# Performance work log

Measured on AMD Instinct MI355X. Metric: run time of the kernel, lower is better.

## Reference

```python
import jax, jax.numpy as jnp
import numpy as np

N_NODES = 50000
EPS = 1e-5


def sage_conv_max(x, src, dst, W_l, b_l, W_r):
    # PyG SAGEConv(aggr='max'): out = lin_l(max_j x_j) + lin_r(x_i)
    msg = x[src]                                   # [E, d] gather
    agg = jnp.full((x.shape[0], x.shape[1]), -jnp.inf, dtype=x.dtype)
    agg = agg.at[dst].max(msg)                     # scatter-max over edges
    agg = jnp.where(jnp.isneginf(agg), 0.0, agg)   # isolated nodes -> 0 (PyG convention)
    return agg @ W_l.T + b_l + x @ W_r.T


def batch_norm(x, gamma, beta):
    mean = jnp.mean(x, axis=0)
    var = jnp.var(x, axis=0)
    return (x - mean) * jax.lax.rsqrt(var + EPS) * gamma + beta


def setup_inputs() -> dict:
    key = jax.random.key(0)
    ks = jax.random.split(key, 10)
    d_in, d_h, d_out = 128, 128, 32
    s = lambda fan: 1.0 / np.sqrt(fan)
    return {
        "x": jax.random.normal(ks[0], (N_NODES, d_in), dtype=jnp.float32),
        "edge_index": jax.random.randint(ks[1], (2, 800000), 0, N_NODES, dtype=jnp.int32),
        "W_l1": jax.random.uniform(ks[2], (d_h, d_in), jnp.float32, -s(d_in), s(d_in)),
        "b_l1": jnp.zeros((d_h,), jnp.float32),
        "W_r1": jax.random.uniform(ks[3], (d_h, d_in), jnp.float32, -s(d_in), s(d_in)),
        "gamma1": jnp.ones((d_h,), jnp.float32),
        "beta1": jnp.zeros((d_h,), jnp.float32),
        "W_l2": jax.random.uniform(ks[4], (d_out, d_h), jnp.float32, -s(d_h), s(d_h)),
        "b_l2": jnp.zeros((d_out,), jnp.float32),
        "W_r2": jax.random.uniform(ks[5], (d_out, d_h), jnp.float32, -s(d_h), s(d_h)),
    }


def reference(x, edge_index, W_l1, b_l1, W_r1, gamma1, beta1, W_l2, b_l2, W_r2):
    src, dst = edge_index[0], edge_index[1]
    h = sage_conv_max(x, src, dst, W_l1, b_l1, W_r1)
    h = batch_norm(h, gamma1, beta1)
    h = jax.nn.relu(h)
    # dropout is identity at inference
    return sage_conv_max(h, src, dst, W_l2, b_l2, W_r2)
```

## Files before the change

kernel.cpp:

```cpp
#include <hip/hip_runtime.h>
#include <math.h>
#include <float.h>

#define N_NODES 50000
#define N_EDGES 800000
#define NB 196
#define EB 4096
#define NBUCK 98
#define BSH 9
#define CAP 80
#define SEGC 9216
#define CELLS_PER_BUCKET (NB * CAP)
#define GCHUNKS 784
#define GGRID (GCHUNKS * 4)

typedef __attribute__((ext_vector_type(8))) short bf16x8;
typedef __attribute__((ext_vector_type(4))) float f32x4;

static __device__ __forceinline__ unsigned short f2bf(float f) {
  unsigned int u = __float_as_uint(f);
  u = (u + 0x7fff + ((u >> 16) & 1)) >> 16;
  return (unsigned short)u;
}

__global__ __launch_bounds__(256) void setup_kernel(
    const int* __restrict__ src, const int* __restrict__ dst,
    unsigned int* __restrict__ pairs,
    const float* __restrict__ x, const float* __restrict__ Wl1,
    const float* __restrict__ Wr1, const float* __restrict__ Wl2,
    const float* __restrict__ Wr2, unsigned int* __restrict__ x_bf,
    unsigned short* __restrict__ Wcat1, unsigned short* __restrict__ Wcat2,
    float* __restrict__ gsums) {
  const int b = blockIdx.x, tid = threadIdx.x;
  if (b < NB) {
    __shared__ unsigned int lp[NBUCK * CAP];
    __shared__ int cur[NBUCK];
    for (int s = tid; s < NBUCK * CAP; s += 256) lp[s] = 0x80000000u;
    if (tid < NBUCK) cur[tid] = 0;
    __syncthreads();
#pragma unroll
    for (int it = 0; it < EB / 256; ++it) {
      int e = b * EB + it * 256 + tid;
      if (e < N_EDGES) {
        int d = dst[e];
        int bk = d >> BSH;
        int p = atomicAdd(&cur[bk], 1);
        if (p < CAP)
          lp[bk * CAP + p] = (unsigned)src[e] | ((unsigned)(d & 511) << 16);
      }
    }
    __syncthreads();
    for (int s = tid; s < NBUCK * CAP; s += 256) {
      int bk = s / CAP, p = s - bk * CAP;
      pairs[(size_t)(bk * NB + b) * CAP + p] = lp[s];
    }
  } else if (b < NB + 6250) {
    int i = (b - NB) * 256 + tid;
    float4 v = ((const float4*)x)[i];
    uint2 o;
    o.x = (unsigned int)f2bf(v.x) | ((unsigned int)f2bf(v.y) << 16);
    o.y = (unsigned int)f2bf(v.z) | ((unsigned int)f2bf(v.w) << 16);
    ((uint2*)x_bf)[i] = o;
  } else if (b < NB + 6410) {
    int i = (b - NB - 6250) * 256 + tid;
    if (i < 32768) {
      int n = i >> 8, k = i & 255;
      float w = (k < 128) ? Wl1[n * 128 + k] : Wr1[n * 128 + (k - 128)];
      Wcat1[i] = f2bf(w);
    } else if (i < 40960) {
      int j = i - 32768;
      int n = j >> 8, k = j & 255;
      float w = (k < 128) ? Wl2[n * 128 + k] : Wr2[n * 128 + (k - 128)];
      Wcat2[j] = f2bf(w);
    }
  } else {
#pragma unroll
    for (int i = 0; i < 8; ++i) gsums[i * 256 + tid] = 0.f;
  }
}

__global__ __launch_bounds__(1024) void bucket_sort(const unsigned int* __restrict__ pairs,
                                                    unsigned int* __restrict__ rowinfo,
                                                    int* __restrict__ elist) {
  __shared__ int hist[512], cpos[512];
  __shared__ int wsum[8];
  const int b = blockIdx.x, tid = threadIdx.x;
  const size_t s0 = (size_t)b * CELLS_PER_BUCKET;
  if (tid < 512) hist[tid] = 0;
  __syncthreads();
  for (int p = tid; p < CELLS_PER_BUCKET; p += 1024) {
    unsigned int pr = pairs[s0 + p];
    if ((int)pr >= 0) atomicAdd(&hist[(pr >> 16) & 511], 1);
  }
  __syncthreads();
  int incl = 0, h = 0;
  if (tid < 512) {
    const int l = tid & 63;
    h = hist[tid];
    incl = h;
#pragma unroll
    for (int off = 1; off < 64; off <<= 1) {
      int t = __shfl_up(incl, off, 64);
      if (l >= off) incl += t;
    }
    if (l == 63) wsum[tid >> 6] = incl;
  }
  __syncthreads();
  if (tid < 64) {
    int v = (tid < 8) ? wsum[tid] : 0;
#pragma unroll
    for (int off = 1; off < 8; off <<= 1) {
      int t = __shfl_up(v, off, 64);
      if (tid >= off) v += t;
    }
    if (tid < 8) wsum[tid] = v;
  }
  __syncthreads();
  if (tid < 512) {
    const int w = tid >> 6;
    int tot = incl + ((w > 0) ? wsum[w - 1] : 0);
    int excl = tot - h;
    cpos[tid] = excl;
    int node = (b << BSH) + tid;
    if (node < N_NODES)
      rowinfo[node] = (unsigned)(b * SEGC + excl) | ((unsigned)h << 20);
  }
  __syncthreads();
  for (int p = tid; p < CELLS_PER_BUCKET; p += 1024) {
    unsigned int pr = pairs[s0 + p];
    if ((int)pr >= 0) {
      int loc = atomicAdd(&cpos[(pr >> 16) & 511], 1);
      elist[b * SEGC + loc] = (int)(pr & 0xffffu);
    }
  }
}

template <bool BN>
__global__ __launch_bounds__(256) void gather_slice(
    const unsigned int* __restrict__ feat,
    const unsigned int* __restrict__ rowinfo,
    const int* __restrict__ elist,
    const float* __restrict__ gsums,
    const float* __restrict__ gamma, const float* __restrict__ beta,
    unsigned int* __restrict__ out) {
  __shared__ float s_scale[32], s_shift[32];
  const int bid = blockIdx.x;
  const int grp = bid & 7;
  const int slice = grp >> 1;
  const int chunk = ((bid >> 3) << 1) + (grp & 1);
  const int tid = threadIdx.x;
  if (BN) {
    if (tid < 32) {
      int f = slice * 32 + tid;
      float sm = 0.f, sq = 0.f;
#pragma unroll
      for (int r = 0; r < 8; ++r) {
        sm += gsums[r * 256 + f];
        sq += gsums[r * 256 + 128 + f];
      }
      const float inv = 1.f / (float)N_NODES;
      float mean = sm * inv;
      float var = sq * inv - mean * mean;
      float sc = gamma[f] * rsqrtf(var + 1e-5f);
      s_scale[tid] = sc;
      s_shift[tid] = beta[f] - mean * sc;
    }
    __syncthreads();
  }
  const int g = tid >> 4;
  const int fq = tid & 15;
  const unsigned int* fs = feat + slice * 16 + fq;
#pragma unroll
  for (int it = 0; it < 4; ++it) {
    int node = chunk * 64 + it * 16 + g;
    if (node >= N_NODES) node = N_NODES - 1;
    unsigned int info = rowinfo[node];
    int e0 = (int)(info & 0xFFFFFu);
    int deg = (int)(info >> 20);
    float m0, m1;
    if (deg > 0) {
      m0 = -FLT_MAX; m1 = -FLT_MAX;
      const int last = e0 + deg - 1;
      for (int base = e0; base <= last; base += 4) {
        int idx[4];
#pragma unroll
        for (int q = 0; q < 4; ++q) {
          int e = base + q;
          if (e > last) e = last;
          idx[q] = elist[e];
        }
        unsigned int v[4];
#pragma unroll
        for (int q = 0; q < 4; ++q) v[q] = fs[(size_t)idx[q] * 64];
#pragma unroll
        for (int q = 0; q < 4; ++q) {
          m0 = fmaxf(m0, __uint_as_float(v[q] << 16));
          m1 = fmaxf(m1, __uint_as_float(v[q] & 0xffff0000u));
        }
      }
      if (BN) {
        m0 = fmaxf(m0 * s_scale[2 * fq] + s_shift[2 * fq], 0.f);
        m1 = fmaxf(m1 * s_scale[2 * fq + 1] + s_shift[2 * fq + 1], 0.f);
      }
    } else {
      m0 = 0.f; m1 = 0.f;
    }
    out[(size_t)node * 64 + slice * 16 + fq] =
        (unsigned)f2bf(m0) | ((unsigned)f2bf(m1) << 16);
  }
}

#define ASTR 264

template <int NT, bool BF16OUT, bool STATS, bool BNIN>
__global__ __launch_bounds__(256) void gemm_mfma(
    const unsigned short* __restrict__ Aa, const unsigned short* __restrict__ Ab,
    const unsigned short* __restrict__ Wcat, const float* __restrict__ bias,
    unsigned short* __restrict__ outb, float* __restrict__ outf,
    float* __restrict__ gsums, const float* __restrict__ gamma,
    const float* __restrict__ beta, int N) {
  __shared__ unsigned short Alds[128 * ASTR];
  __shared__ float s_sum[128], s_sq[128];
  __shared__ float s_scale[128], s_shift[128];
  const int tid = threadIdx.x;
  const int rowBase = blockIdx.x * 128;

  if (STATS && tid < 128) { s_sum[tid] = 0.f; s_sq[tid] = 0.f; }
  if (BNIN) {
    if (tid < 128) {
      float sm = 0.f, sq = 0.f;
#pragma unroll
      for (int r = 0; r < 8; ++r) {
        sm += gsums[r * 256 + tid];
        sq += gsums[r * 256 + 128 + tid];
      }
      const float inv = 1.f / (float)N_NODES;
      float mean = sm * inv;
      float var = sq * inv - mean * mean;
      float sc = gamma[tid] * rsqrtf(var + 1e-5f);
      s_scale[tid] = sc;
      s_shift[tid] = beta[tid] - mean * sc;
    }
    __syncthreads();
  }

#pragma unroll
  for (int it = 0; it < 16; ++it) {
    int f = tid + it * 256;
    int r = f >> 5;
    int seg = f & 31;
    int n = rowBase + r;
    if (n >= N) n = N - 1;
    const unsigned short* src = (seg < 16)
        ? (Aa + (size_t)n * 128 + seg * 8)
        : (Ab + (size_t)n * 128 + (seg - 16) * 8);
    int4 d = *(const int4*)src;
    if (BNIN && seg >= 16) {
      int kb = (seg - 16) * 8;
      unsigned int* dp = (unsigned int*)&d;
#pragma unroll
      for (int c = 0; c < 4; ++c) {
        int k0 = kb + 2 * c;
        float lo = __uint_as_float(dp[c] << 16);
        float hi = __uint_as_float(dp[c] & 0xffff0000u);
        lo = fmaxf(lo * s_scale[k0] + s_shift[k0], 0.f);
        hi = fmaxf(hi * s_scale[k0 + 1] + s_shift[k0 + 1], 0.f);
        dp[c] = (unsigned)f2bf(lo) | ((unsigned)f2bf(hi) << 16);
      }
    }
    *(int4*)(&Alds[r * ASTR + seg * 8]) = d;
  }
  __syncthreads();

  const int wv = tid >> 6;
  const int lane = tid & 63;
  const int ln15 = lane & 15;
  const int quad = lane >> 4;
  const int m0 = wv * 32;

  f32x4 acc[2][NT] = {};

#pragma unroll
  for (int ks = 0; ks < 8; ++ks) {
    const int k0 = ks * 32;
    bf16x8 a0 = *(const bf16x8*)(&Alds[(m0 + ln15) * ASTR + k0 + quad * 8]);
    bf16x8 a1 = *(const bf16x8*)(&Alds[(m0 + 16 + ln15) * ASTR + k0 + quad * 8]);
#pragma unroll
    for (int nt = 0; nt < NT; ++nt) {
      bf16x8 b = *(const bf16x8*)(Wcat + (size_t)(nt * 16 + ln15) * 256 + k0 + quad * 8);
      acc[0][nt] = __builtin_amdgcn_mfma_f32_16x16x32_bf16(a0, b, acc[0][nt], 0, 0, 0);
      acc[1][nt] = __builtin_amdgcn_mfma_f32_16x16x32_bf16(a1, b, acc[1][nt], 0, 0, 0);
    }
  }

  const int ldo = NT * 16;
#pragma unroll
  for (int nt = 0; nt < NT; ++nt) {
    int col = nt * 16 + ln15;
    float bv = bias[col];
    float psum = 0.f, psq = 0.f;
#pragma unroll
    for (int mt = 0; mt < 2; ++mt) {
#pragma unroll
      for (int i = 0; i < 4; ++i) {
        int r = rowBase + m0 + mt * 16 + quad * 4 + i;
        if (r < N) {
          float val = acc[mt][nt][i] + bv;
          if (STATS) { psum += val; psq += val * val; }
          if (BF16OUT)
            outb[(size_t)r * ldo + col] = f2bf(val);
          else
            outf[(size_t)r * ldo + col] = val;
        }
      }
    }
    if (STATS) {
      atomicAdd(&s_sum[col], psum);
      atomicAdd(&s_sq[col], psq);
    }
  }
  if (STATS) {
    __syncthreads();
    if (tid < 128) {
      int rep = blockIdx.x & 7;
      atomicAdd(&gsums[rep * 256 + tid], s_sum[tid]);
      atomicAdd(&gsums[rep * 256 + 128 + tid], s_sq[tid]);
    }
  }
}

extern "C" void kernel_launch(void* const* d_in, const int* in_sizes, int n_in,
                              void* d_out, int out_size, void* d_ws, size_t ws_size,
                              hipStream_t stream) {
  (void)in_sizes; (void)n_in; (void)out_size; (void)ws_size;
  const float* x     = (const float*)d_in[0];
  const int*   eidx  = (const int*)d_in[1];
  const float* W_l1  = (const float*)d_in[2];
  const float* b_l1  = (const float*)d_in[3];
  const float* W_r1  = (const float*)d_in[4];
  const float* gamma = (const float*)d_in[5];
  const float* beta  = (const float*)d_in[6];
  const float* W_l2  = (const float*)d_in[7];
  const float* b_l2  = (const float*)d_in[8];
  const float* W_r2  = (const float*)d_in[9];
  const int* srcp = eidx;
  const int* dstp = eidx + N_EDGES;
  float* out = (float*)d_out;

  int* wsi = (int*)d_ws;
  float* gsums   = (float*)wsi;
  unsigned int* rowinfo = (unsigned int*)(wsi + 2048);
  int*   elist   = wsi + 52064;
  unsigned int* pairs   = (unsigned int*)(wsi + 955232);
  unsigned int* x_bf    = (unsigned int*)(wsi + 2491872);
  unsigned int* agg_bf  = (unsigned int*)(wsi + 5691872);
  unsigned int* h_bf    = (unsigned int*)(wsi + 8891872);
  unsigned short* Wcat1 = (unsigned short*)(wsi + 12091872);
  unsigned short* Wcat2 = (unsigned short*)(wsi + 12108256);

  setup_kernel<<<dim3(NB + 6410 + 1), 256, 0, stream>>>(
      srcp, dstp, pairs, x, W_l1, W_r1, W_l2, W_r2, x_bf, Wcat1, Wcat2, gsums);

  bucket_sort<<<dim3(NBUCK), 1024, 0, stream>>>(pairs, rowinfo, elist);

  gather_slice<false><<<dim3(GGRID), 256, 0, stream>>>(
      x_bf, rowinfo, elist, nullptr, nullptr, nullptr, agg_bf);

  gemm_mfma<8, true, true, false><<<dim3(391), 256, 0, stream>>>(
      (const unsigned short*)agg_bf, (const unsigned short*)x_bf, Wcat1, b_l1,
      (unsigned short*)h_bf, nullptr, gsums, nullptr, nullptr, N_NODES);

  gather_slice<true><<<dim3(GGRID), 256, 0, stream>>>(
      h_bf, rowinfo, elist, gsums, gamma, beta, agg_bf);

  gemm_mfma<2, false, false, true><<<dim3(391), 256, 0, stream>>>(
      (const unsigned short*)agg_bf, (const unsigned short*)h_bf, Wcat2, b_l2,
      nullptr, out, gsums, gamma, beta, N_NODES);
}
```

Before: 246.5 us.

## Replace two-pass bucket sort with global-atomic degree count, scan, and placement

Builds the CSR edge list with a different method. A global atomic degree histogram is filled in the setup kernel, a per-bucket scan produces row offsets, and a placement kernel scatters each edge's source with atomic decrements. This drops the intermediate pairs buffer and the low-parallelism 98-block sort kernel, and it removes the CAP overflow limit. In exchange it adds a memset, an extra kernel launch, contended global atomics, and edge order within a row that is no longer fixed. The gather block-to-slice mapping also changes so that all chunks of one slice are contiguous in block ID.

```diff
diff --git a/kernel.cpp b/kernel.cpp
--- a/kernel.cpp
+++ b/kernel.cpp
@@ -3,16 +3,14 @@
 #include <float.h>
 
 #define N_NODES 50000
+#define N_PAD 50176
 #define N_EDGES 800000
-#define NB 196
-#define EB 4096
 #define NBUCK 98
 #define BSH 9
-#define CAP 80
 #define SEGC 9216
-#define CELLS_PER_BUCKET (NB * CAP)
 #define GCHUNKS 784
 #define GGRID (GCHUNKS * 4)
+#define CNT_BLKS 3125
 
 typedef __attribute__((ext_vector_type(8))) short bf16x8;
 typedef __attribute__((ext_vector_type(4))) float f32x4;
@@ -24,45 +22,25 @@
 }
 
 __global__ __launch_bounds__(256) void setup_kernel(
-    const int* __restrict__ src, const int* __restrict__ dst,
-    unsigned int* __restrict__ pairs,
+    const int* __restrict__ dst, int* __restrict__ deg,
     const float* __restrict__ x, const float* __restrict__ Wl1,
     const float* __restrict__ Wr1, const float* __restrict__ Wl2,
     const float* __restrict__ Wr2, unsigned int* __restrict__ x_bf,
     unsigned short* __restrict__ Wcat1, unsigned short* __restrict__ Wcat2,
     float* __restrict__ gsums) {
   const int b = blockIdx.x, tid = threadIdx.x;
-  if (b < NB) {
-    __shared__ unsigned int lp[NBUCK * CAP];
-    __shared__ int cur[NBUCK];
-    for (int s = tid; s < NBUCK * CAP; s += 256) lp[s] = 0x80000000u;
-    if (tid < NBUCK) cur[tid] = 0;
-    __syncthreads();
-#pragma unroll
-    for (int it = 0; it < EB / 256; ++it) {
-      int e = b * EB + it * 256 + tid;
-      if (e < N_EDGES) {
-        int d = dst[e];
-        int bk = d >> BSH;
-        int p = atomicAdd(&cur[bk], 1);
-        if (p < CAP)
-          lp[bk * CAP + p] = (unsigned)src[e] | ((unsigned)(d & 511) << 16);
-      }
-    }
-    __syncthreads();
-    for (int s = tid; s < NBUCK * CAP; s += 256) {
-      int bk = s / CAP, p = s - bk * CAP;
-      pairs[(size_t)(bk * NB + b) * CAP + p] = lp[s];
-    }
-  } else if (b < NB + 6250) {
-    int i = (b - NB) * 256 + tid;
+  if (b < CNT_BLKS) {
+    int e = b * 256 + tid;
+    atomicAdd(&deg[dst[e]], 1);
+  } else if (b < CNT_BLKS + 6250) {
+    int i = (b - CNT_BLKS) * 256 + tid;
     float4 v = ((const float4*)x)[i];
     uint2 o;
     o.x = (unsigned int)f2bf(v.x) | ((unsigned int)f2bf(v.y) << 16);
     o.y = (unsigned int)f2bf(v.z) | ((unsigned int)f2bf(v.w) << 16);
     ((uint2*)x_bf)[i] = o;
-  } else if (b < NB + 6410) {
-    int i = (b - NB - 6250) * 256 + tid;
+  } else if (b < CNT_BLKS + 6410) {
+    int i = (b - CNT_BLKS - 6250) * 256 + tid;
     if (i < 32768) {
       int n = i >> 8, k = i & 255;
       float w = (k < 128) ? Wl1[n * 128 + k] : Wr1[n * 128 + (k - 128)];
@@ -79,32 +57,20 @@
   }
 }
 
-__global__ __launch_bounds__(1024) void bucket_sort(const unsigned int* __restrict__ pairs,
-                                                    unsigned int* __restrict__ rowinfo,
-                                                    int* __restrict__ elist) {
-  __shared__ int hist[512], cpos[512];
+__global__ __launch_bounds__(512) void scan_deg(const int* __restrict__ deg,
+                                                unsigned int* __restrict__ rowinfo) {
   __shared__ int wsum[8];
   const int b = blockIdx.x, tid = threadIdx.x;
-  const size_t s0 = (size_t)b * CELLS_PER_BUCKET;
-  if (tid < 512) hist[tid] = 0;
-  __syncthreads();
-  for (int p = tid; p < CELLS_PER_BUCKET; p += 1024) {
-    unsigned int pr = pairs[s0 + p];
-    if ((int)pr >= 0) atomicAdd(&hist[(pr >> 16) & 511], 1);
-  }
-  __syncthreads();
-  int incl = 0, h = 0;
-  if (tid < 512) {
-    const int l = tid & 63;
-    h = hist[tid];
-    incl = h;
-#pragma unroll
-    for (int off = 1; off < 64; off <<= 1) {
-      int t = __shfl_up(incl, off, 64);
-      if (l >= off) incl += t;
-    }
-    if (l == 63) wsum[tid >> 6] = incl;
-  }
+  const int node = (b << BSH) + tid;
+  const int d = deg[node];
+  const int l = tid & 63;
+  int incl = d;
+#pragma unroll
+  for (int off = 1; off < 64; off <<= 1) {
+    int t = __shfl_up(incl, off, 64);
+    if (l >= off) incl += t;
+  }
+  if (l == 63) wsum[tid >> 6] = incl;
   __syncthreads();
   if (tid < 64) {
     int v = (tid < 8) ? wsum[tid] : 0;
@@ -116,23 +82,20 @@
     if (tid < 8) wsum[tid] = v;
   }
   __syncthreads();
-  if (tid < 512) {
-    const int w = tid >> 6;
-    int tot = incl + ((w > 0) ? wsum[w - 1] : 0);
-    int excl = tot - h;
-    cpos[tid] = excl;
-    int node = (b << BSH) + tid;
-    if (node < N_NODES)
-      rowinfo[node] = (unsigned)(b * SEGC + excl) | ((unsigned)h << 20);
-  }
-  __syncthreads();
-  for (int p = tid; p < CELLS_PER_BUCKET; p += 1024) {
-    unsigned int pr = pairs[s0 + p];
-    if ((int)pr >= 0) {
-      int loc = atomicAdd(&cpos[(pr >> 16) & 511], 1);
-      elist[b * SEGC + loc] = (int)(pr & 0xffffu);
-    }
-  }
+  const int w = tid >> 6;
+  int excl = incl - d + ((w > 0) ? wsum[w - 1] : 0);
+  rowinfo[node] = (unsigned)(b * SEGC + excl) | ((unsigned)d << 20);
+}
+
+__global__ __launch_bounds__(256) void place_edges(
+    const int* __restrict__ src, const int* __restrict__ dst,
+    const unsigned int* __restrict__ rowinfo, int* __restrict__ deg,
+    int* __restrict__ elist) {
+  int e = blockIdx.x * 256 + threadIdx.x;
+  int s = src[e], d = dst[e];
+  int e0 = (int)(rowinfo[d] & 0xFFFFFu);
+  int p = atomicAdd(&deg[d], -1) - 1;
+  elist[e0 + p] = s;
 }
 
 template <bool BN>
@@ -145,9 +108,8 @@
     unsigned int* __restrict__ out) {
   __shared__ float s_scale[32], s_shift[32];
   const int bid = blockIdx.x;
-  const int grp = bid & 7;
-  const int slice = grp >> 1;
-  const int chunk = ((bid >> 3) << 1) + (grp & 1);
+  const int slice = bid / GCHUNKS;
+  const int chunk = bid - slice * GCHUNKS;
   const int tid = threadIdx.x;
   if (BN) {
     if (tid < 32) {
@@ -350,18 +312,22 @@
   int* wsi = (int*)d_ws;
   float* gsums   = (float*)wsi;
   unsigned int* rowinfo = (unsigned int*)(wsi + 2048);
-  int*   elist   = wsi + 52064;
-  unsigned int* pairs   = (unsigned int*)(wsi + 955232);
-  unsigned int* x_bf    = (unsigned int*)(wsi + 2491872);
-  unsigned int* agg_bf  = (unsigned int*)(wsi + 5691872);
-  unsigned int* h_bf    = (unsigned int*)(wsi + 8891872);
-  unsigned short* Wcat1 = (unsigned short*)(wsi + 12091872);
-  unsigned short* Wcat2 = (unsigned short*)(wsi + 12108256);
-
-  setup_kernel<<<dim3(NB + 6410 + 1), 256, 0, stream>>>(
-      srcp, dstp, pairs, x, W_l1, W_r1, W_l2, W_r2, x_bf, Wcat1, Wcat2, gsums);
-
-  bucket_sort<<<dim3(NBUCK), 1024, 0, stream>>>(pairs, rowinfo, elist);
+  int*   deg     = wsi + 52224;
+  int*   elist   = wsi + 102400;
+  unsigned int* x_bf    = (unsigned int*)(wsi + 1005568);
+  unsigned int* agg_bf  = (unsigned int*)(wsi + 4205568);
+  unsigned int* h_bf    = (unsigned int*)(wsi + 7405568);
+  unsigned short* Wcat1 = (unsigned short*)(wsi + 10605568);
+  unsigned short* Wcat2 = (unsigned short*)(wsi + 10621952);
+
+  hipMemsetAsync(deg, 0, N_PAD * sizeof(int), stream);
+
+  setup_kernel<<<dim3(CNT_BLKS + 6410 + 1), 256, 0, stream>>>(
+      dstp, deg, x, W_l1, W_r1, W_l2, W_r2, x_bf, Wcat1, Wcat2, gsums);
+
+  scan_deg<<<dim3(NBUCK), 512, 0, stream>>>(deg, rowinfo);
+
+  place_edges<<<dim3(CNT_BLKS), 256, 0, stream>>>(srcp, dstp, rowinfo, deg, elist);
 
   gather_slice<false><<<dim3(GGRID), 256, 0, stream>>>(
       x_bf, rowinfo, elist, nullptr, nullptr, nullptr, agg_bf);
```

Measured after the change: 299.2 us. 21.4% more time.

## Halve bucket width, write edge pairs directly, and track per-cell counts

Applied to the files above, without the earlier changes.

Doubles the number of edge blocks and destination buckets (256 nodes per bucket, smaller per-cell capacity). The setup kernel now writes packed src/dst pairs straight to global memory and records per-cell fill counts, instead of staging them in LDS and flushing a sentinel-filled buffer. The bucket sort reads the counts and skips empty slots. The gather grid mapping also changes from interleaved slice/chunk to slice-major. The aim is less LDS initialisation and copying, less sentinel traffic, and more parallelism in sorting. The risks are uncoalesced scattered global writes and a smaller capacity margin per cell, which could drop edges if a cell overflows.

```diff
diff --git a/kernel.cpp b/kernel.cpp
--- a/kernel.cpp
+++ b/kernel.cpp
@@ -4,12 +4,12 @@
 
 #define N_NODES 50000
 #define N_EDGES 800000
-#define NB 196
-#define EB 4096
-#define NBUCK 98
-#define BSH 9
-#define CAP 80
-#define SEGC 9216
+#define NB 392
+#define EB 2048
+#define NBUCK 196
+#define BSH 8
+#define CAP 36
+#define SEGC 4864
 #define CELLS_PER_BUCKET (NB * CAP)
 #define GCHUNKS 784
 #define GGRID (GCHUNKS * 4)
@@ -25,7 +25,7 @@
 
 __global__ __launch_bounds__(256) void setup_kernel(
     const int* __restrict__ src, const int* __restrict__ dst,
-    unsigned int* __restrict__ pairs,
+    unsigned int* __restrict__ pairs, int* __restrict__ counts,
     const float* __restrict__ x, const float* __restrict__ Wl1,
     const float* __restrict__ Wr1, const float* __restrict__ Wl2,
     const float* __restrict__ Wr2, unsigned int* __restrict__ x_bf,
@@ -33,9 +33,7 @@
     float* __restrict__ gsums) {
   const int b = blockIdx.x, tid = threadIdx.x;
   if (b < NB) {
-    __shared__ unsigned int lp[NBUCK * CAP];
     __shared__ int cur[NBUCK];
-    for (int s = tid; s < NBUCK * CAP; s += 256) lp[s] = 0x80000000u;
     if (tid < NBUCK) cur[tid] = 0;
     __syncthreads();
 #pragma unroll
@@ -46,13 +44,14 @@
         int bk = d >> BSH;
         int p = atomicAdd(&cur[bk], 1);
         if (p < CAP)
-          lp[bk * CAP + p] = (unsigned)src[e] | ((unsigned)(d & 511) << 16);
-      }
-    }
-    __syncthreads();
-    for (int s = tid; s < NBUCK * CAP; s += 256) {
-      int bk = s / CAP, p = s - bk * CAP;
-      pairs[(size_t)(bk * NB + b) * CAP + p] = lp[s];
+          pairs[(size_t)(bk * NB + b) * CAP + p] =
+              (unsigned)src[e] | ((unsigned)(d & 255) << 16);
+      }
+    }
+    __syncthreads();
+    if (tid < NBUCK) {
+      int c = cur[tid];
+      counts[tid * NB + b] = c > CAP ? CAP : c;
     }
   } else if (b < NB + 6250) {
     int i = (b - NB) * 256 + tid;
@@ -80,21 +79,26 @@
 }
 
 __global__ __launch_bounds__(1024) void bucket_sort(const unsigned int* __restrict__ pairs,
+                                                    const int* __restrict__ counts,
                                                     unsigned int* __restrict__ rowinfo,
                                                     int* __restrict__ elist) {
-  __shared__ int hist[512], cpos[512];
-  __shared__ int wsum[8];
+  __shared__ int hist[256], cpos[256], cnt[NB];
+  __shared__ int wsum[4];
   const int b = blockIdx.x, tid = threadIdx.x;
   const size_t s0 = (size_t)b * CELLS_PER_BUCKET;
-  if (tid < 512) hist[tid] = 0;
+  if (tid < 256) hist[tid] = 0;
+  if (tid < NB) cnt[tid] = counts[b * NB + tid];
   __syncthreads();
   for (int p = tid; p < CELLS_PER_BUCKET; p += 1024) {
-    unsigned int pr = pairs[s0 + p];
-    if ((int)pr >= 0) atomicAdd(&hist[(pr >> 16) & 511], 1);
+    int c = p / CAP, s = p - c * CAP;
+    if (s < cnt[c]) {
+      unsigned int pr = pairs[s0 + p];
+      atomicAdd(&hist[(pr >> 16) & 255], 1);
+    }
   }
   __syncthreads();
   int incl = 0, h = 0;
-  if (tid < 512) {
+  if (tid < 256) {
     const int l = tid & 63;
     h = hist[tid];
     incl = h;
@@ -107,16 +111,16 @@
   }
   __syncthreads();
   if (tid < 64) {
-    int v = (tid < 8) ? wsum[tid] : 0;
-#pragma unroll
-    for (int off = 1; off < 8; off <<= 1) {
+    int v = (tid < 4) ? wsum[tid] : 0;
+#pragma unroll
+    for (int off = 1; off < 4; off <<= 1) {
       int t = __shfl_up(v, off, 64);
       if (tid >= off) v += t;
     }
-    if (tid < 8) wsum[tid] = v;
-  }
-  __syncthreads();
-  if (tid < 512) {
+    if (tid < 4) wsum[tid] = v;
+  }
+  __syncthreads();
+  if (tid < 256) {
     const int w = tid >> 6;
     int tot = incl + ((w > 0) ? wsum[w - 1] : 0);
     int excl = tot - h;
@@ -127,9 +131,10 @@
   }
   __syncthreads();
   for (int p = tid; p < CELLS_PER_BUCKET; p += 1024) {
-    unsigned int pr = pairs[s0 + p];
-    if ((int)pr >= 0) {
-      int loc = atomicAdd(&cpos[(pr >> 16) & 511], 1);
+    int c = p / CAP, s = p - c * CAP;
+    if (s < cnt[c]) {
+      unsigned int pr = pairs[s0 + p];
+      int loc = atomicAdd(&cpos[(pr >> 16) & 255], 1);
       elist[b * SEGC + loc] = (int)(pr & 0xffffu);
     }
   }
@@ -145,9 +150,8 @@
     unsigned int* __restrict__ out) {
   __shared__ float s_scale[32], s_shift[32];
   const int bid = blockIdx.x;
-  const int grp = bid & 7;
-  const int slice = grp >> 1;
-  const int chunk = ((bid >> 3) << 1) + (grp & 1);
+  const int slice = bid / GCHUNKS;
+  const int chunk = bid - slice * GCHUNKS;
   const int tid = threadIdx.x;
   if (BN) {
     if (tid < 32) {
@@ -350,29 +354,28 @@
   int* wsi = (int*)d_ws;
   float* gsums   = (float*)wsi;
   unsigned int* rowinfo = (unsigned int*)(wsi + 2048);
-  int*   elist   = wsi + 52064;
-  unsigned int* pairs   = (unsigned int*)(wsi + 955232);
-  unsigned int* x_bf    = (unsigned int*)(wsi + 2491872);
-  unsigned int* agg_bf  = (unsigned int*)(wsi + 5691872);
-  unsigned int* h_bf    = (unsigned int*)(wsi + 8891872);
-  unsigned short* Wcat1 = (unsigned short*)(wsi + 12091872);
-  unsigned short* Wcat2 = (unsigned short*)(wsi + 12108256);
+  int*   counts  = wsi + 52224;
+  int*   elist   = wsi + 129056;
+  unsigned int* pairs   = (unsigned int*)(wsi + 1082400);
+  unsigned int* x_bf    = (unsigned int*)(wsi + 3848352);
+  unsigned int* agg_bf  = (unsigned int*)(wsi + 7048352);
+  unsigned int* h_bf    = (unsigned int*)(wsi + 10248352);
+  unsigned short* Wcat1 = (unsigned short*)(wsi + 13448352);
+  unsigned short* Wcat2 = (unsigned short*)(wsi + 13464736);
 
   setup_kernel<<<dim3(NB + 6410 + 1), 256, 0, stream>>>(
-      srcp, dstp, pairs, x, W_l1, W_r1, W_l2, W_r2, x_bf, Wcat1, Wcat2, gsums);
-
-  bucket_sort<<<dim3(NBUCK), 1024, 0, stream>>>(pairs, rowinfo, elist);
+      srcp, dstp, pairs, counts, x, W_l1, W_r1, W_l2, W_r2, x_bf, Wcat1, Wcat2, gsums);
+
+  bucket_sort<<<dim3(NBUCK), 1024, 0, stream>>>(pairs, counts, rowinfo, elist);
 
   gather_slice<false><<<dim3(GGRID), 256, 0, stream>>>(
       x_bf, rowinfo, elist, nullptr, nullptr, nullptr, agg_bf);
-
   gemm_mfma<8, true, true, false><<<dim3(391), 256, 0, stream>>>(
       (const unsigned short*)agg_bf, (const unsigned short*)x_bf, Wcat1, b_l1,
       (unsigned short*)h_bf, nullptr, gsums, nullptr, nullptr, N_NODES);
 
   gather_slice<true><<<dim3(GGRID), 256, 0, stream>>>(
       h_bf, rowinfo, elist, gsums, gamma, beta, agg_bf);
-
   gemm_mfma<2, false, false, true><<<dim3(391), 256, 0, stream>>>(
       (const unsigned short*)agg_bf, (const unsigned short*)h_bf, Wcat2, b_l2,
       nullptr, out, gsums, gamma, beta, N_NODES);
```

Result: faster. 240.9 us (-2.3%).
